# Kernel tuning notes

Measured on AMD Instinct MI355X. Metric: run time of the kernel, lower is better.

The kernel has to match this reference:

```python
import jax, jax.numpy as jnp
import numpy as np

C, H, W = 3, 224, 224
P = 14  # patches per row
PS = H // P  # 16
PATCH_DIM = C * PS * PS  # 768
HIDDEN = 768


def patchify(images):
    # images: [n, c, h, w] -> [n, P*P, c*PS*PS], flatten order (c, ph, pw)
    n = images.shape[0]
    x = images.reshape(n, C, P, PS, P, PS)
    x = x.transpose(0, 2, 4, 1, 3, 5)  # [n, Pi, Pj, c, ps, ps]
    return x.reshape(n, P * P, PATCH_DIM)


def setup_inputs() -> dict:
    key = jax.random.key(0)
    k1, k2, k3 = jax.random.split(key, 3)
    images = jax.random.normal(k1, (128, C, H, W), dtype=jnp.float32)
    # nn.Linear(patch_embedding_dim, hidden_dim): weight [out, in], bias [out]
    bound = 1.0 / np.sqrt(PATCH_DIM)
    W_lin = jax.random.uniform(k2, (HIDDEN, PATCH_DIM), minval=-bound, maxval=bound, dtype=jnp.float32)
    b_lin = jax.random.uniform(k3, (HIDDEN,), minval=-bound, maxval=bound, dtype=jnp.float32)
    cls_token = jnp.ones((1, HIDDEN), dtype=jnp.float32)
    return {"images": images, "W_lin": W_lin, "b_lin": b_lin, "cls_token": cls_token}


def reference(images, W_lin, b_lin, cls_token):
    patches = patchify(images)                        # [n, 196, 768]
    hidden = jnp.einsum('npd,hd->nph', patches, W_lin) + b_lin  # [n, 196, H]
    n = images.shape[0]
    cls = jnp.broadcast_to(cls_token[None], (n, 1, HIDDEN))
    return jnp.concatenate([cls, hidden], axis=1)     # [n, 197, H]
```

## Files before the change

kernel.cpp:

```cpp
#include <hip/hip_runtime.h>
#include <cstdint>


#define PGRID 14
#define PSZ   16
#define CHN   3
#define IMGW  224
#define KDIM  768
#define NDIM  768
#define NPATCH 196

typedef short bf16x8 __attribute__((ext_vector_type(8)));
typedef short short8v __attribute__((ext_vector_type(8)));
typedef float f32x4  __attribute__((ext_vector_type(4)));

__device__ __forceinline__ short bf16rne(float f) {
    uint32_t u = __builtin_bit_cast(uint32_t, f);
    u += 0x7FFFu + ((u >> 16) & 1u);
    return (short)(u >> 16);
}

__device__ __forceinline__ short8v cvt8(float4 v0, float4 v1) {
    short8v s;
    s[0] = bf16rne(v0.x); s[1] = bf16rne(v0.y); s[2] = bf16rne(v0.z); s[3] = bf16rne(v0.w);
    s[4] = bf16rne(v1.x); s[5] = bf16rne(v1.y); s[6] = bf16rne(v1.z); s[7] = bf16rne(v1.w);
    return s;
}

__global__ __launch_bounds__(256) void prep_patch(
    const float* __restrict__ img, short* __restrict__ A, int M)
{
    int t = blockIdx.x * 256 + threadIdx.x;
    if (t >= M * 96) return;
    int m  = t / 96;
    int k8 = t - m * 96;
    int k  = k8 * 8;
    int c  = k >> 8;
    int ph = (k >> 4) & 15;
    int pw = k & 15;
    int im = m / NPATCH;
    int p  = m - im * NPATCH;
    int Pi = p / PGRID;
    int Pj = p - Pi * PGRID;
    const float* src = img + (((long)(im * CHN + c) * IMGW + Pi * PSZ + ph) * IMGW + Pj * PSZ + pw);
    float4 v0 = *(const float4*)src;
    float4 v1 = *(const float4*)(src + 4);
    *(short8v*)(A + (long)m * KDIM + k) = cvt8(v0, v1);
}

__global__ __launch_bounds__(256) void prep_small(
    const float* __restrict__ Wl, const float* __restrict__ cls,
    short* __restrict__ Wb, float* __restrict__ out, int n_img)
{
    int t = blockIdx.x * 256 + threadIdx.x;
    const int WCH = KDIM * NDIM / 8;
    if (t < WCH) {
        float4 v0 = *(const float4*)(Wl + (long)t * 8);
        float4 v1 = *(const float4*)(Wl + (long)t * 8 + 4);
        *(short8v*)(Wb + (long)t * 8) = cvt8(v0, v1);
    } else {
        int u = t - WCH;
        if (u < n_img * 96) {
            int im = u / 96;
            int k8 = u - im * 96;
            float4 v0 = *(const float4*)(cls + k8 * 8);
            float4 v1 = *(const float4*)(cls + k8 * 8 + 4);
            float* dst = out + (long)im * 197 * NDIM + k8 * 8;
            *(float4*)dst = v0;
            *(float4*)(dst + 4) = v1;
        }
    }
}

__global__ __launch_bounds__(256) void vit_gemm3(
    const short* __restrict__ A, const short* __restrict__ B,
    const float* __restrict__ bias, float* __restrict__ out,
    int M, int mgroups)
{
    {
    }
    const int bid = blockIdx.x;
    const int xcd = bid & 7;
    const int s   = bid >> 3;
    const int gq  = s / 6;
    const int j   = s - gq * 6;
    const int g   = gq * 8 + xcd;
    if (g >= mgroups) return;
    const int m0 = g * 128;
    const int n0 = j * 128;

    __shared__ short As[128 * 64];
    __shared__ short Bs[128 * 64];

    const int tid = threadIdx.x;
    const int wave = tid >> 6;
    const int lane = tid & 63;

    const int srow = tid >> 3;
    const int sk   = (tid & 7) ^ (srow & 7);
    const long abase = (long)(m0 + srow) * KDIM + sk * 8;
    const long bbase = (long)(n0 + srow) * KDIM + sk * 8;

    const int wm = (wave & 1) * 64;
    const int wn = (wave >> 1) * 64;
    const int wq = lane >> 4;
    const int lr = lane & 15;
    const int blk0 = ((wq)     ^ (lr & 7)) * 8;
    const int blk1 = ((wq + 4) ^ (lr & 7)) * 8;

    f32x4 acc[4][4] = {};
    bf16x8 ra[4], rb[4];

    #pragma unroll
    for (int jj = 0; jj < 4; ++jj) {
        ra[jj] = *(const bf16x8*)(A + abase + (long)jj * 32 * KDIM);
        rb[jj] = *(const bf16x8*)(B + bbase + (long)jj * 32 * KDIM);
    }

    for (int kk = 0; kk < KDIM; kk += 64) {
        #pragma unroll
        for (int jj = 0; jj < 4; ++jj) {
            *(bf16x8*)(&As[(jj * 256 + tid) * 8]) = ra[jj];
            *(bf16x8*)(&Bs[(jj * 256 + tid) * 8]) = rb[jj];
        }
        __syncthreads();

        if (kk + 64 < KDIM) {
            #pragma unroll
            for (int jj = 0; jj < 4; ++jj) {
                ra[jj] = *(const bf16x8*)(A + abase + (long)jj * 32 * KDIM + kk + 64);
                rb[jj] = *(const bf16x8*)(B + bbase + (long)jj * 32 * KDIM + kk + 64);
            }
        }

        #pragma unroll
        for (int ks = 0; ks < 2; ++ks) {
            const int blk = ks ? blk1 : blk0;
            bf16x8 a[4], b[4];
            #pragma unroll
            for (int i = 0; i < 4; ++i)
                a[i] = *(const bf16x8*)(&As[(wm + i * 16 + lr) * 64 + blk]);
            #pragma unroll
            for (int i = 0; i < 4; ++i)
                b[i] = *(const bf16x8*)(&Bs[(wn + i * 16 + lr) * 64 + blk]);
            #pragma unroll
            for (int i = 0; i < 4; ++i)
                #pragma unroll
                for (int jm = 0; jm < 4; ++jm)
                    acc[i][jm] = __builtin_amdgcn_mfma_f32_16x16x32_bf16(a[i], b[jm], acc[i][jm], 0, 0, 0);
        }
        __syncthreads();
    }

    float bv[4];
    #pragma unroll
    for (int jm = 0; jm < 4; ++jm) bv[jm] = bias[n0 + wn + jm * 16 + lr];

    #pragma unroll
    for (int i = 0; i < 4; ++i) {
        #pragma unroll
        for (int r = 0; r < 4; ++r) {
            int gm = m0 + wm + i * 16 + wq * 4 + r;
            if (gm < M) {
                int im = gm / NPATCH;
                int p  = gm - im * NPATCH;
                long orow = ((long)im * 197 + 1 + p) * (long)NDIM;
                #pragma unroll
                for (int jm = 0; jm < 4; ++jm)
                    out[orow + n0 + wn + jm * 16 + lr] = acc[i][jm][r] + bv[jm];
            }
        }
    }
}

#define LDSTR 40
__global__ __launch_bounds__(256) void vit_gemm_fb(
    const float* __restrict__ img, const float* __restrict__ Wl,
    const float* __restrict__ bias, float* __restrict__ out, int n_img)
{
    const int M = n_img * NPATCH;
    __shared__ short As[128 * LDSTR];
    __shared__ short Bs[128 * LDSTR];
    const int tid = threadIdx.x;
    const int m0 = blockIdx.y * 128;
    const int n0 = blockIdx.x * 128;
    const int col4  = tid & 7;
    const int rbase = tid >> 3;
    long arow[4];
    for (int rr = 0; rr < 4; ++rr) {
        int m = m0 + rbase + rr * 32;
        int mm = (m < M) ? m : (M - 1);
        int im = mm / NPATCH;
        int p  = mm % NPATCH;
        int Pi = p / PGRID;
        int Pj = p % PGRID;
        arow[rr] = ((long)(im * CHN) * IMGW + Pi * PSZ) * IMGW + Pj * PSZ;
    }
    const int lane = tid & 63;
    const int wave = tid >> 6;
    const int wm = (wave & 1) * 64;
    const int wn = (wave >> 1) * 64;
    const int wq = lane >> 4;
    const int lr = lane & 15;
    f32x4 acc[4][4] = {};
    for (int k0 = 0; k0 < KDIM; k0 += 32) {
        {
            int k  = k0 + col4 * 4;
            int c  = k >> 8;
            int ph = (k >> 4) & 15;
            int pw = k & 15;
            long koff = (long)(c * IMGW + ph) * IMGW + pw;
            #pragma unroll
            for (int rr = 0; rr < 4; ++rr) {
                const float4 v = *(const float4*)(img + arow[rr] + koff);
                int row = rbase + rr * 32;
                short4 s;
                s.x = bf16rne(v.x); s.y = bf16rne(v.y);
                s.z = bf16rne(v.z); s.w = bf16rne(v.w);
                *(short4*)(&As[row * LDSTR + col4 * 4]) = s;
            }
        }
        {
            int k = k0 + col4 * 4;
            #pragma unroll
            for (int rr = 0; rr < 4; ++rr) {
                int nrow = rbase + rr * 32;
                const float4 v = *(const float4*)(Wl + (long)(n0 + nrow) * KDIM + k);
                short4 s;
                s.x = bf16rne(v.x); s.y = bf16rne(v.y);
                s.z = bf16rne(v.z); s.w = bf16rne(v.w);
                *(short4*)(&Bs[nrow * LDSTR + col4 * 4]) = s;
            }
        }
        __syncthreads();
        bf16x8 a[4], b[4];
        #pragma unroll
        for (int i = 0; i < 4; ++i)
            a[i] = *(const bf16x8*)(&As[(wm + i * 16 + lr) * LDSTR + wq * 8]);
        #pragma unroll
        for (int i = 0; i < 4; ++i)
            b[i] = *(const bf16x8*)(&Bs[(wn + i * 16 + lr) * LDSTR + wq * 8]);
        #pragma unroll
        for (int i = 0; i < 4; ++i)
            #pragma unroll
            for (int j = 0; j < 4; ++j)
                acc[i][j] = __builtin_amdgcn_mfma_f32_16x16x32_bf16(a[i], b[j], acc[i][j], 0, 0, 0);
        __syncthreads();
    }
    float bv[4];
    #pragma unroll
    for (int j = 0; j < 4; ++j) bv[j] = bias[n0 + wn + j * 16 + lr];
    #pragma unroll
    for (int i = 0; i < 4; ++i) {
        #pragma unroll
        for (int r = 0; r < 4; ++r) {
            int gm = m0 + wm + i * 16 + wq * 4 + r;
            if (gm < M) {
                int im = gm / NPATCH;
                int p  = gm % NPATCH;
                long orow = ((long)im * 197 + 1 + p) * (long)NDIM;
                #pragma unroll
                for (int j = 0; j < 4; ++j)
                    out[orow + n0 + wn + j * 16 + lr] = acc[i][j][r] + bv[j];
            }
        }
    }
}

__global__ __launch_bounds__(256) void cls_fill(
    const float* __restrict__ cls, float* __restrict__ out, int n_img)
{
    int i = blockIdx.x * 256 + threadIdx.x;
    if (i < n_img * NDIM) {
        int im = i / NDIM;
        int n  = i - im * NDIM;
        out[(long)im * 197 * NDIM + n] = cls[n];
    }
}

extern "C" void kernel_launch(void* const* d_in, const int* in_sizes, int n_in,
                              void* d_out, int out_size, void* d_ws, size_t ws_size,
                              hipStream_t stream) {
    const float* img  = (const float*)d_in[0];
    const float* Wl   = (const float*)d_in[1];
    const float* bias = (const float*)d_in[2];
    const float* cls  = (const float*)d_in[3];
    float* out = (float*)d_out;

    int n_img = in_sizes[0] / (CHN * IMGW * IMGW);
    int M = n_img * NPATCH;
    int mgroups = (M + 127) / 128;
    long Mpad = (long)mgroups * 128;

    size_t need = (size_t)(Mpad * KDIM + (long)KDIM * NDIM) * sizeof(short);
    if (ws_size >= need) {
        short* A_ws = (short*)d_ws;
        short* Wb   = A_ws + Mpad * KDIM;

        prep_patch<<<(M * 96 + 255) / 256, 256, 0, stream>>>(img, A_ws, M);
        int small_total = KDIM * NDIM / 8 + n_img * 96;
        prep_small<<<(small_total + 255) / 256, 256, 0, stream>>>(Wl, cls, Wb, out, n_img);

        int gpad = (mgroups + 7) & ~7;
        int nblocks = gpad * 6;
        vit_gemm3<<<nblocks, 256, 0, stream>>>(A_ws, Wb, bias, out, M, mgroups);
    } else {
        dim3 grid(NDIM / 128, mgroups);
        vit_gemm_fb<<<grid, 256, 0, stream>>>(img, Wl, bias, out, n_img);
        int cls_elems = n_img * NDIM;
        cls_fill<<<(cls_elems + 255) / 256, 256, 0, stream>>>(cls, out, n_img);
    }
}
```

Baseline: 181.4 us.

## Pre-swizzle GEMM operands into MFMA fragment layout and drop LDS staging

```diff
diff --git a/kernel.cpp b/kernel.cpp
--- a/kernel.cpp
+++ b/kernel.cpp
@@ -9,6 +9,7 @@
 #define KDIM  768
 #define NDIM  768
 #define NPATCH 196
+#define K32   24
 
 typedef short bf16x8 __attribute__((ext_vector_type(8)));
 typedef short short8v __attribute__((ext_vector_type(8)));
@@ -45,7 +46,11 @@
     const float* src = img + (((long)(im * CHN + c) * IMGW + Pi * PSZ + ph) * IMGW + Pj * PSZ + pw);
     float4 v0 = *(const float4*)src;
     float4 v1 = *(const float4*)(src + 4);
-    *(short8v*)(A + (long)m * KDIM + k) = cvt8(v0, v1);
+    int m16  = m >> 4;
+    int k32  = k8 >> 2;
+    int quad = k8 & 3;
+    int lane = (m & 15) | (quad << 4);
+    *(short8v*)(A + (((long)m16 * K32 + k32) << 9) + lane * 8) = cvt8(v0, v1);
 }
 
 __global__ __launch_bounds__(256) void prep_small(
@@ -55,9 +60,15 @@
     int t = blockIdx.x * 256 + threadIdx.x;
     const int WCH = KDIM * NDIM / 8;
     if (t < WCH) {
-        float4 v0 = *(const float4*)(Wl + (long)t * 8);
-        float4 v1 = *(const float4*)(Wl + (long)t * 8 + 4);
-        *(short8v*)(Wb + (long)t * 8) = cvt8(v0, v1);
+        int n  = t / 96;
+        int k8 = t - n * 96;
+        float4 v0 = *(const float4*)(Wl + (long)n * KDIM + k8 * 8);
+        float4 v1 = *(const float4*)(Wl + (long)n * KDIM + k8 * 8 + 4);
+        int n16  = n >> 4;
+        int k32  = k8 >> 2;
+        int quad = k8 & 3;
+        int lane = (n & 15) | (quad << 4);
+        *(short8v*)(Wb + (((long)n16 * K32 + k32) << 9) + lane * 8) = cvt8(v0, v1);
     } else {
         int u = t - WCH;
         if (u < n_img * 96) {
@@ -72,13 +83,11 @@
     }
 }
 
-__global__ __launch_bounds__(256) void vit_gemm3(
+__global__ __launch_bounds__(256, 2) void vit_gemm4(
     const short* __restrict__ A, const short* __restrict__ B,
     const float* __restrict__ bias, float* __restrict__ out,
     int M, int mgroups)
 {
-    {
-    }
     const int bid = blockIdx.x;
     const int xcd = bid & 7;
     const int s   = bid >> 3;
@@ -86,88 +95,58 @@
     const int j   = s - gq * 6;
     const int g   = gq * 8 + xcd;
     if (g >= mgroups) return;
-    const int m0 = g * 128;
+    const int m0 = g * 256;
     const int n0 = j * 128;
 
-    __shared__ short As[128 * 64];
-    __shared__ short Bs[128 * 64];
-
-    const int tid = threadIdx.x;
+    const int tid  = threadIdx.x;
     const int wave = tid >> 6;
     const int lane = tid & 63;
-
-    const int srow = tid >> 3;
-    const int sk   = (tid & 7) ^ (srow & 7);
-    const long abase = (long)(m0 + srow) * KDIM + sk * 8;
-    const long bbase = (long)(n0 + srow) * KDIM + sk * 8;
-
-    const int wm = (wave & 1) * 64;
-    const int wn = (wave >> 1) * 64;
-    const int wq = lane >> 4;
-    const int lr = lane & 15;
-    const int blk0 = ((wq)     ^ (lr & 7)) * 8;
-    const int blk1 = ((wq + 4) ^ (lr & 7)) * 8;
-
-    f32x4 acc[4][4] = {};
-    bf16x8 ra[4], rb[4];
-
-    #pragma unroll
-    for (int jj = 0; jj < 4; ++jj) {
-        ra[jj] = *(const bf16x8*)(A + abase + (long)jj * 32 * KDIM);
-        rb[jj] = *(const bf16x8*)(B + bbase + (long)jj * 32 * KDIM);
-    }
-
-    for (int kk = 0; kk < KDIM; kk += 64) {
-        #pragma unroll
-        for (int jj = 0; jj < 4; ++jj) {
-            *(bf16x8*)(&As[(jj * 256 + tid) * 8]) = ra[jj];
-            *(bf16x8*)(&Bs[(jj * 256 + tid) * 8]) = rb[jj];
-        }
-        __syncthreads();
-
-        if (kk + 64 < KDIM) {
-            #pragma unroll
-            for (int jj = 0; jj < 4; ++jj) {
-                ra[jj] = *(const bf16x8*)(A + abase + (long)jj * 32 * KDIM + kk + 64);
-                rb[jj] = *(const bf16x8*)(B + bbase + (long)jj * 32 * KDIM + kk + 64);
-            }
-        }
-
-        #pragma unroll
-        for (int ks = 0; ks < 2; ++ks) {
-            const int blk = ks ? blk1 : blk0;
-            bf16x8 a[4], b[4];
-            #pragma unroll
-            for (int i = 0; i < 4; ++i)
-                a[i] = *(const bf16x8*)(&As[(wm + i * 16 + lr) * 64 + blk]);
-            #pragma unroll
-            for (int i = 0; i < 4; ++i)
-                b[i] = *(const bf16x8*)(&Bs[(wn + i * 16 + lr) * 64 + blk]);
-            #pragma unroll
-            for (int i = 0; i < 4; ++i)
-                #pragma unroll
-                for (int jm = 0; jm < 4; ++jm)
-                    acc[i][jm] = __builtin_amdgcn_mfma_f32_16x16x32_bf16(a[i], b[jm], acc[i][jm], 0, 0, 0);
-        }
-        __syncthreads();
-    }
-
-    float bv[4];
-    #pragma unroll
-    for (int jm = 0; jm < 4; ++jm) bv[jm] = bias[n0 + wn + jm * 16 + lr];
-
+    const int wq   = lane >> 4;
+    const int lr   = lane & 15;
+
+    const short* Ab = A + (((long)((m0 >> 4) + wave * 4) * K32) << 9) + lane * 8;
+    const short* Bb = B + (((long)(n0 >> 4) * K32) << 9) + lane * 8;
+    const long fstride = (long)K32 << 9;
+
+    f32x4 acc[4][8] = {};
+    bf16x8 a0[4], b0[8], a1[4], b1[8];
+
+#define LDA(dst, kk) { _Pragma("unroll") for (int i = 0; i < 4; ++i) \
+        dst[i] = *(const bf16x8*)(Ab + i * fstride + ((kk) << 9)); }
+#define LDB(dst, kk) { _Pragma("unroll") for (int i = 0; i < 8; ++i) \
+        dst[i] = *(const bf16x8*)(Bb + i * fstride + ((kk) << 9)); }
+#define MM(aa, bb) { _Pragma("unroll") for (int i = 0; i < 4; ++i) \
+        _Pragma("unroll") for (int q = 0; q < 8; ++q) \
+        acc[i][q] = __builtin_amdgcn_mfma_f32_16x16x32_bf16(aa[i], bb[q], acc[i][q], 0, 0, 0); }
+
+    LDA(a0, 0); LDB(b0, 0);
+    for (int k = 0; k < K32; k += 2) {
+        LDA(a1, k + 1); LDB(b1, k + 1);
+        MM(a0, b0);
+        if (k + 2 < K32) { LDA(a0, k + 2); LDB(b0, k + 2); }
+        MM(a1, b1);
+    }
+#undef LDA
+#undef LDB
+#undef MM
+
+    float bv[8];
+    #pragma unroll
+    for (int q = 0; q < 8; ++q) bv[q] = bias[n0 + q * 16 + lr];
+
+    const int mw = m0 + wave * 64;
     #pragma unroll
     for (int i = 0; i < 4; ++i) {
         #pragma unroll
         for (int r = 0; r < 4; ++r) {
-            int gm = m0 + wm + i * 16 + wq * 4 + r;
+            int gm = mw + i * 16 + wq * 4 + r;
             if (gm < M) {
                 int im = gm / NPATCH;
                 int p  = gm - im * NPATCH;
-                long orow = ((long)im * 197 + 1 + p) * (long)NDIM;
+                float* orow = out + ((long)im * 197 + 1 + p) * NDIM + n0 + lr;
                 #pragma unroll
-                for (int jm = 0; jm < 4; ++jm)
-                    out[orow + n0 + wn + jm * 16 + lr] = acc[i][jm][r] + bv[jm];
+                for (int q = 0; q < 8; ++q)
+                    orow[q * 16] = acc[i][q][r] + bv[q];
             }
         }
     }
@@ -289,8 +268,8 @@
 
     int n_img = in_sizes[0] / (CHN * IMGW * IMGW);
     int M = n_img * NPATCH;
-    int mgroups = (M + 127) / 128;
-    long Mpad = (long)mgroups * 128;
+    int mgroups = (M + 255) / 256;
+    long Mpad = (long)mgroups * 256;
 
     size_t need = (size_t)(Mpad * KDIM + (long)KDIM * NDIM) * sizeof(short);
     if (ws_size >= need) {
@@ -303,9 +282,10 @@
 
         int gpad = (mgroups + 7) & ~7;
         int nblocks = gpad * 6;
-        vit_gemm3<<<nblocks, 256, 0, stream>>>(A_ws, Wb, bias, out, M, mgroups);
+        vit_gemm4<<<nblocks, 256, 0, stream>>>(A_ws, Wb, bias, out, M, mgroups);
     } else {
-        dim3 grid(NDIM / 128, mgroups);
+        int mb = (M + 127) / 128;
+        dim3 grid(NDIM / 128, mb);
         vit_gemm_fb<<<grid, 256, 0, stream>>>(img, Wl, bias, out, n_img);
         int cls_elems = n_img * NDIM;
         cls_fill<<<(cls_elems + 255) / 256, 256, 0, stream>>>(cls, out, n_img);
```

New measurement: 190.5 us. 5.0% more time.
